# Optimization experiments

Measured on AMD Instinct MI355X. Metric: run time of the kernel, lower is better.

## Reference

```python
import jax, jax.numpy as jnp
import numpy as np

B, T, H, F = 32, 2048, 1024, 1024  # batch, kv_len, hidden_size, feature_size


def setup_inputs() -> dict:
    key = jax.random.key(0)
    ks = jax.random.split(key, 6)
    s = 0.02  # param init scale
    return {
        "query": jax.random.normal(ks[0], (B, 1, H), jnp.float32),
        "keys": jax.random.normal(ks[1], (B, T, F), jnp.float32),
        "Wa_w": jax.random.normal(ks[2], (H, H), jnp.float32) * s,
        "Wa_b": jnp.zeros((H,), jnp.float32),
        "Ua_w": jax.random.normal(ks[3], (H, F), jnp.float32) * s,
        "Ua_b": jnp.zeros((H,), jnp.float32),
        "Va_w": jax.random.normal(ks[4], (1, H), jnp.float32) * s,
        "Va_b": jnp.zeros((1,), jnp.float32),
    }


def reference(query, keys, Wa_w, Wa_b, Ua_w, Ua_b, Va_w, Va_b):
    # Wa(query): [B,1,H]; Ua(keys): [B,T,H]
    q = jnp.einsum('bqh,oh->bqo', query, Wa_w) + Wa_b
    k = jnp.einsum('btf,of->bto', keys, Ua_w) + Ua_b
    e = jnp.tanh(q + k)                                   # [B,T,H] (broadcast over q dim of size 1)
    scores = jnp.einsum('bth,h->bt', e, Va_w[0]) + Va_b[0]  # Va(...).squeeze(2) -> [B,T]
    scores = scores[:, None, :]                           # unsqueeze(1) -> [B,1,T]
    weights = jax.nn.softmax(scores, axis=-1)             # [B,1,T]
    context = jnp.einsum('bqt,btf->bqf', weights, keys)   # bmm -> [B,1,F]
    return context, weights
```

## Files before the change

kernel.cpp:

```cpp
#include <hip/hip_runtime.h>
#include <hip/hip_bf16.h>

typedef float  f32x4 __attribute__((ext_vector_type(4)));
typedef short  s16x8 __attribute__((ext_vector_type(8)));
typedef __hip_bfloat16 bf16;

#define BDIM 32
#define TDIM 2048
#define HDIM 1024
#define FDIM 1024
#define MTOT (BDIM*TDIM)

#define GLOAD16(gp, lp) __builtin_amdgcn_global_load_lds(                     \
    (const __attribute__((address_space(1))) void*)(gp),                      \
    (__attribute__((address_space(3))) void*)(lp), 16, 0, 0)

#define MFMA_BF16 __builtin_amdgcn_mfma_f32_16x16x32_bf16

__global__ __launch_bounds__(256) void cvt_bf16_kernel(
    const float* __restrict__ src, bf16* __restrict__ dst, int n8)
{
    int i = blockIdx.x * 256 + threadIdx.x;
    const int stride = gridDim.x * 256;
    for (; i < n8; i += stride) {
        const f32x4 a = ((const f32x4*)src)[2 * i];
        const f32x4 b = ((const f32x4*)src)[2 * i + 1];
        union { bf16 h[8]; s16x8 v; } u;
        #pragma unroll
        for (int j = 0; j < 4; ++j) {
            u.h[j]     = __float2bfloat16(a[j]);
            u.h[4 + j] = __float2bfloat16(b[j]);
        }
        ((s16x8*)dst)[i] = u.v;
    }
}

__global__ __launch_bounds__(256) void qeff_kernel(
    const float* __restrict__ query, const float* __restrict__ Wa_w,
    const float* __restrict__ Wa_b,  const float* __restrict__ Ua_b,
    float* __restrict__ qe)
{
    const int lane = threadIdx.x & 63;
    const int gw   = blockIdx.x * 4 + (threadIdx.x >> 6);
    const int b    = gw >> 10;
    const int o    = gw & 1023;
    const float* qp = query + (size_t)b * HDIM;
    const float* wp = Wa_w  + (size_t)o * HDIM;
    float s = 0.f;
    #pragma unroll
    for (int i = 0; i < 16; ++i) {
        const int h = i * 64 + lane;
        s += qp[h] * wp[h];
    }
    #pragma unroll
    for (int off = 32; off > 0; off >>= 1) s += __shfl_down(s, off);
    if (lane == 0) qe[gw] = s + Wa_b[o] + Ua_b[o];
}

#define STAGE_A(buf_, kb_, h_, s_) GLOAD16(                                    \
    Ab + (size_t)(M0 + (h_)*128 + (((s_)>>1)<<4) + srow) * FDIM               \
       + (kb_) + (((s_)&1)<<5) + scg*8,                                        \
    &As[buf_][((((h_)*8 + ((s_)>>1)) * 2 + ((s_)&1)) << 9)])
#define STAGE_B(buf_, kb_, h_, s_) GLOAD16(                                    \
    Bb + (size_t)(N0 + (h_)*128 + (((s_)>>1)<<4) + srow) * FDIM               \
       + (kb_) + (((s_)&1)<<5) + scg*8,                                        \
    &Bs[buf_][((((h_)*8 + ((s_)>>1)) * 2 + ((s_)&1)) << 9)])

__global__ __launch_bounds__(512) void score_gemm_256_kernel(
    const bf16* __restrict__ Ab, const bf16* __restrict__ Bb,
    const float* __restrict__ qe, const float* __restrict__ Va,
    float* __restrict__ scores)
{
    __shared__ bf16 As[2][16384];
    __shared__ bf16 Bs[2][16384];

    const int tid  = threadIdx.x;
    const int lane = tid & 63;
    const int w    = tid >> 6;
    const int wr   = w >> 2;
    const int wc   = w & 3;

    const int bid   = blockIdx.x;
    const int local = bid >> 3;
    const int mt    = (bid & 7) * 32 + (local >> 2);
    const int nt    = local & 3;
    const int M0 = mt * 256, N0 = nt * 256;

    const int srow = lane >> 2;
    const int scg  = (lane & 3) ^ (((lane >> 5) & 1) << 1);
    const int r    = lane & 15;
    const int q4   = lane >> 4;
    const int roff = r * 32 + ((q4 ^ (((r >> 3) & 1) << 1)) & 3) * 8;

    f32x4 acc[8][4];
    #pragma unroll
    for (int m = 0; m < 8; ++m)
        #pragma unroll
        for (int n = 0; n < 4; ++n) acc[m][n] = (f32x4){0.f, 0.f, 0.f, 0.f};

    STAGE_B(0, 0, 0, w); STAGE_B(0, 0, 0, w + 8);
    STAGE_B(0, 0, 1, w); STAGE_B(0, 0, 1, w + 8);
    STAGE_A(0, 0, 0, w); STAGE_A(0, 0, 0, w + 8);
    STAGE_A(0, 0, 1, w); STAGE_A(0, 0, 1, w + 8);
    STAGE_B(1, 64, 0, w); STAGE_B(1, 64, 0, w + 8);
    STAGE_B(1, 64, 1, w); STAGE_B(1, 64, 1, w + 8);
    asm volatile("s_waitcnt vmcnt(4)" ::: "memory");
    __builtin_amdgcn_s_barrier();

    for (int i = 0; i < 8; ++i) {
        const bool pf   = (i < 7);
        const int kbO1 = (2 * i + 1) << 6;
        const int kbE2 = (2 * i + 2) << 6;
        const int kbO2 = (2 * i + 3) << 6;

        s16x8 a0[4][2], a1[4][2], b0[2][2], b1[2][2];

        #pragma unroll
        for (int mf = 0; mf < 4; ++mf)
            #pragma unroll
            for (int ks = 0; ks < 2; ++ks)
                a0[mf][ks] = *(const s16x8*)
                    &As[0][(((wr * 8 + mf) * 2 + ks) << 9) + roff];
        #pragma unroll
        for (int nf = 0; nf < 2; ++nf)
            #pragma unroll
            for (int ks = 0; ks < 2; ++ks)
                b0[nf][ks] = *(const s16x8*)
                    &Bs[0][(((wc * 4 + nf) * 2 + ks) << 9) + roff];
        STAGE_A(1, kbO1, 0, w); STAGE_A(1, kbO1, 0, w + 8);
        __builtin_amdgcn_s_barrier();
        __builtin_amdgcn_s_setprio(1);
        #pragma unroll
        for (int mf = 0; mf < 4; ++mf)
            #pragma unroll
            for (int nf = 0; nf < 2; ++nf)
                #pragma unroll
                for (int ks = 0; ks < 2; ++ks)
                    acc[mf][nf] = MFMA_BF16(a0[mf][ks], b0[nf][ks],
                                            acc[mf][nf], 0, 0, 0);
        __builtin_amdgcn_s_setprio(0);
        __builtin_amdgcn_s_barrier();

        #pragma unroll
        for (int nf = 0; nf < 2; ++nf)
            #pragma unroll
            for (int ks = 0; ks < 2; ++ks)
                b1[nf][ks] = *(const s16x8*)
                    &Bs[0][(((wc * 4 + 2 + nf) * 2 + ks) << 9) + roff];
        STAGE_A(1, kbO1, 1, w); STAGE_A(1, kbO1, 1, w + 8);
        __builtin_amdgcn_s_barrier();
        __builtin_amdgcn_s_setprio(1);
        #pragma unroll
        for (int mf = 0; mf < 4; ++mf)
            #pragma unroll
            for (int nf = 0; nf < 2; ++nf)
                #pragma unroll
                for (int ks = 0; ks < 2; ++ks)
                    acc[mf][2 + nf] = MFMA_BF16(a0[mf][ks], b1[nf][ks],
                                                acc[mf][2 + nf], 0, 0, 0);
        __builtin_amdgcn_s_setprio(0);
        __builtin_amdgcn_s_barrier();

        #pragma unroll
        for (int mf = 0; mf < 4; ++mf)
            #pragma unroll
            for (int ks = 0; ks < 2; ++ks)
                a1[mf][ks] = *(const s16x8*)
                    &As[0][(((wr * 8 + 4 + mf) * 2 + ks) << 9) + roff];
        if (pf) { STAGE_B(0, kbE2, 0, w); STAGE_B(0, kbE2, 0, w + 8); }
        __builtin_amdgcn_s_barrier();
        __builtin_amdgcn_s_setprio(1);
        #pragma unroll
        for (int mf = 0; mf < 4; ++mf)
            #pragma unroll
            for (int nf = 0; nf < 2; ++nf)
                #pragma unroll
                for (int ks = 0; ks < 2; ++ks)
                    acc[4 + mf][nf] = MFMA_BF16(a1[mf][ks], b0[nf][ks],
                                                acc[4 + mf][nf], 0, 0, 0);
        __builtin_amdgcn_s_setprio(0);
        __builtin_amdgcn_s_barrier();

        if (pf) { STAGE_B(0, kbE2, 1, w); STAGE_B(0, kbE2, 1, w + 8); }
        __builtin_amdgcn_s_barrier();
        __builtin_amdgcn_s_setprio(1);
        #pragma unroll
        for (int mf = 0; mf < 4; ++mf)
            #pragma unroll
            for (int nf = 0; nf < 2; ++nf)
                #pragma unroll
                for (int ks = 0; ks < 2; ++ks)
                    acc[4 + mf][2 + nf] = MFMA_BF16(a1[mf][ks], b1[nf][ks],
                                                    acc[4 + mf][2 + nf], 0, 0, 0);
        __builtin_amdgcn_s_setprio(0);
        if (pf) asm volatile("s_waitcnt vmcnt(4)" ::: "memory");
        else    asm volatile("s_waitcnt vmcnt(0)" ::: "memory");
        __builtin_amdgcn_s_barrier();
        __builtin_amdgcn_sched_barrier(0);

        #pragma unroll
        for (int mf = 0; mf < 4; ++mf)
            #pragma unroll
            for (int ks = 0; ks < 2; ++ks)
                a0[mf][ks] = *(const s16x8*)
                    &As[1][(((wr * 8 + mf) * 2 + ks) << 9) + roff];
        #pragma unroll
        for (int nf = 0; nf < 2; ++nf)
            #pragma unroll
            for (int ks = 0; ks < 2; ++ks)
                b0[nf][ks] = *(const s16x8*)
                    &Bs[1][(((wc * 4 + nf) * 2 + ks) << 9) + roff];
        if (pf) { STAGE_A(0, kbE2, 0, w); STAGE_A(0, kbE2, 0, w + 8); }
        __builtin_amdgcn_s_barrier();
        __builtin_amdgcn_s_setprio(1);
        #pragma unroll
        for (int mf = 0; mf < 4; ++mf)
            #pragma unroll
            for (int nf = 0; nf < 2; ++nf)
                #pragma unroll
                for (int ks = 0; ks < 2; ++ks)
                    acc[mf][nf] = MFMA_BF16(a0[mf][ks], b0[nf][ks],
                                            acc[mf][nf], 0, 0, 0);
        __builtin_amdgcn_s_setprio(0);
        __builtin_amdgcn_s_barrier();

        #pragma unroll
        for (int nf = 0; nf < 2; ++nf)
            #pragma unroll
            for (int ks = 0; ks < 2; ++ks)
                b1[nf][ks] = *(const s16x8*)
                    &Bs[1][(((wc * 4 + 2 + nf) * 2 + ks) << 9) + roff];
        if (pf) { STAGE_A(0, kbE2, 1, w); STAGE_A(0, kbE2, 1, w + 8); }
        __builtin_amdgcn_s_barrier();
        __builtin_amdgcn_s_setprio(1);
        #pragma unroll
        for (int mf = 0; mf < 4; ++mf)
            #pragma unroll
            for (int nf = 0; nf < 2; ++nf)
                #pragma unroll
                for (int ks = 0; ks < 2; ++ks)
                    acc[mf][2 + nf] = MFMA_BF16(a0[mf][ks], b1[nf][ks],
                                                acc[mf][2 + nf], 0, 0, 0);
        __builtin_amdgcn_s_setprio(0);
        __builtin_amdgcn_s_barrier();

        #pragma unroll
        for (int mf = 0; mf < 4; ++mf)
            #pragma unroll
            for (int ks = 0; ks < 2; ++ks)
                a1[mf][ks] = *(const s16x8*)
                    &As[1][(((wr * 8 + 4 + mf) * 2 + ks) << 9) + roff];
        if (pf) { STAGE_B(1, kbO2, 0, w); STAGE_B(1, kbO2, 0, w + 8); }
        __builtin_amdgcn_s_barrier();
        __builtin_amdgcn_s_setprio(1);
        #pragma unroll
        for (int mf = 0; mf < 4; ++mf)
            #pragma unroll
            for (int nf = 0; nf < 2; ++nf)
                #pragma unroll
                for (int ks = 0; ks < 2; ++ks)
                    acc[4 + mf][nf] = MFMA_BF16(a1[mf][ks], b0[nf][ks],
                                                acc[4 + mf][nf], 0, 0, 0);
        __builtin_amdgcn_s_setprio(0);
        __builtin_amdgcn_s_barrier();

        if (pf) { STAGE_B(1, kbO2, 1, w); STAGE_B(1, kbO2, 1, w + 8); }
        __builtin_amdgcn_s_barrier();
        __builtin_amdgcn_s_setprio(1);
        #pragma unroll
        for (int mf = 0; mf < 4; ++mf)
            #pragma unroll
            for (int nf = 0; nf < 2; ++nf)
                #pragma unroll
                for (int ks = 0; ks < 2; ++ks)
                    acc[4 + mf][2 + nf] = MFMA_BF16(a1[mf][ks], b1[nf][ks],
                                                    acc[4 + mf][2 + nf], 0, 0, 0);
        __builtin_amdgcn_s_setprio(0);
        if (pf) {
            asm volatile("s_waitcnt vmcnt(4)" ::: "memory");
            __builtin_amdgcn_s_barrier();
            __builtin_amdgcn_sched_barrier(0);
        }
    }

    const int b = M0 >> 11;
    const float* qrow = qe + (size_t)b * HDIM;
    #pragma unroll
    for (int mf = 0; mf < 8; ++mf) {
        float part[4] = {0.f, 0.f, 0.f, 0.f};
        #pragma unroll
        for (int nf = 0; nf < 4; ++nf) {
            const int c    = N0 + wc * 64 + nf * 16 + (lane & 15);
            const float va = Va[c];
            const float qv = qrow[c];
            #pragma unroll
            for (int j = 0; j < 4; ++j) {
                const float x = qv + acc[mf][nf][j];
                const float e = __expf(2.0f * x);
                part[j] += va * (1.0f - 2.0f / (e + 1.0f));
            }
        }
        #pragma unroll
        for (int j = 0; j < 4; ++j)
            #pragma unroll
            for (int off = 1; off < 16; off <<= 1)
                part[j] += __shfl_xor(part[j], off);
        if ((lane & 15) == 0) {
            const int rr = M0 + wr * 128 + mf * 16 + (lane >> 4) * 4;
            #pragma unroll
            for (int j = 0; j < 4; ++j) atomicAdd(&scores[rr + j], part[j]);
        }
    }
}

__global__ __launch_bounds__(256) void score_gemm_f32_kernel(
    const float* __restrict__ keys, const float* __restrict__ Ua,
    const float* __restrict__ qe,   const float* __restrict__ Va,
    float* __restrict__ scores)
{
    __shared__ bf16 Asf[128][40];
    __shared__ bf16 Bsf[128][40];

    const int tid  = threadIdx.x;
    const int lane = tid & 63;
    const int wid  = tid >> 6;
    const int wr   = wid >> 1, wc = wid & 1;
    const int n0   = blockIdx.x * 128;
    const int m0   = blockIdx.y * 128;

    const int srow  = tid >> 1;
    const int shalf = tid & 1;
    const float* gA = keys + (size_t)(m0 + srow) * FDIM + shalf * 16;
    const float* gB = Ua   + (size_t)(n0 + srow) * FDIM + shalf * 16;

    f32x4 acc[4][4];
    #pragma unroll
    for (int m = 0; m < 4; ++m)
        #pragma unroll
        for (int n = 0; n < 4; ++n) acc[m][n] = (f32x4){0.f, 0.f, 0.f, 0.f};

    float4 ra[4], rbv[4];
    #pragma unroll
    for (int i = 0; i < 4; ++i) {
        ra[i]  = ((const float4*)gA)[i];
        rbv[i] = ((const float4*)gB)[i];
    }

    for (int kt = 0; kt < 32; ++kt) {
        __syncthreads();
        {
            union { bf16 h[16]; s16x8 v[2]; } ua, ub;
            #pragma unroll
            for (int i = 0; i < 4; ++i) {
                const float* fa = (const float*)&ra[i];
                const float* fb = (const float*)&rbv[i];
                #pragma unroll
                for (int j = 0; j < 4; ++j) {
                    ua.h[i*4+j] = __float2bfloat16(fa[j]);
                    ub.h[i*4+j] = __float2bfloat16(fb[j]);
                }
            }
            *(s16x8*)&Asf[srow][shalf*16]     = ua.v[0];
            *(s16x8*)&Asf[srow][shalf*16 + 8] = ua.v[1];
            *(s16x8*)&Bsf[srow][shalf*16]     = ub.v[0];
            *(s16x8*)&Bsf[srow][shalf*16 + 8] = ub.v[1];
        }
        __syncthreads();

        if (kt + 1 < 32) {
            const float* pa = gA + (kt + 1) * 32;
            const float* pb = gB + (kt + 1) * 32;
            #pragma unroll
            for (int i = 0; i < 4; ++i) {
                ra[i]  = ((const float4*)pa)[i];
                rbv[i] = ((const float4*)pb)[i];
            }
        }

        s16x8 af[4], bfr[4];
        #pragma unroll
        for (int m = 0; m < 4; ++m)
            af[m] = *(const s16x8*)&Asf[wr*64 + m*16 + (lane & 15)][(lane >> 4) * 8];
        #pragma unroll
        for (int n = 0; n < 4; ++n)
            bfr[n] = *(const s16x8*)&Bsf[wc*64 + n*16 + (lane & 15)][(lane >> 4) * 8];
        #pragma unroll
        for (int m = 0; m < 4; ++m)
            #pragma unroll
            for (int n = 0; n < 4; ++n)
                acc[m][n] = MFMA_BF16(af[m], bfr[n], acc[m][n], 0, 0, 0);
    }

    const int b = m0 >> 11;
    const float* qrow = qe + (size_t)b * HDIM;
    #pragma unroll
    for (int m = 0; m < 4; ++m) {
        float part[4] = {0.f, 0.f, 0.f, 0.f};
        #pragma unroll
        for (int n = 0; n < 4; ++n) {
            const int c    = n0 + wc*64 + n*16 + (lane & 15);
            const float va = Va[c];
            const float qv = qrow[c];
            #pragma unroll
            for (int j = 0; j < 4; ++j) {
                const float x = qv + acc[m][n][j];
                const float e = __expf(2.0f * x);
                part[j] += va * (1.0f - 2.0f / (e + 1.0f));
            }
        }
        #pragma unroll
        for (int j = 0; j < 4; ++j)
            #pragma unroll
            for (int off = 1; off < 16; off <<= 1)
                part[j] += __shfl_xor(part[j], off);
        if ((lane & 15) == 0) {
            const int rr = m0 + wr*64 + m*16 + (lane >> 4) * 4;
            #pragma unroll
            for (int j = 0; j < 4; ++j) atomicAdd(&scores[rr + j], part[j]);
        }
    }
}

__global__ __launch_bounds__(256) void softmax_kernel(float* __restrict__ sw)
{
    const int b    = blockIdx.x;
    const int tid  = threadIdx.x;
    const int lane = tid & 63, wid = tid >> 6;
    __shared__ float red[8];

    float v[8];
    float m = -3.4e38f;
    #pragma unroll
    for (int i = 0; i < 8; ++i) {
        v[i] = sw[b * TDIM + i * 256 + tid];
        m = fmaxf(m, v[i]);
    }
    #pragma unroll
    for (int off = 32; off > 0; off >>= 1) m = fmaxf(m, __shfl_xor(m, off));
    if (lane == 0) red[wid] = m;
    __syncthreads();
    m = fmaxf(fmaxf(red[0], red[1]), fmaxf(red[2], red[3]));

    float s = 0.f;
    #pragma unroll
    for (int i = 0; i < 8; ++i) { v[i] = __expf(v[i] - m); s += v[i]; }
    #pragma unroll
    for (int off = 32; off > 0; off >>= 1) s += __shfl_xor(s, off);
    if (lane == 0) red[4 + wid] = s;
    __syncthreads();
    s = (red[4] + red[5]) + (red[6] + red[7]);

    const float inv = 1.0f / s;
    #pragma unroll
    for (int i = 0; i < 8; ++i) sw[b * TDIM + i * 256 + tid] = v[i] * inv;
}

__global__ __launch_bounds__(256) void context_bf16_kernel(
    const bf16* __restrict__ keys, const float* __restrict__ w,
    float* __restrict__ ctx)
{
    const int tc  = blockIdx.x;
    const int b   = blockIdx.y;
    const int tid = threadIdx.x;
    __shared__ float ws_[128];
    if (tid < 128) ws_[tid] = w[b * TDIM + tc * 128 + tid];
    __syncthreads();

    const bf16* kp = keys + ((size_t)b * TDIM + (size_t)tc * 128) * FDIM + tid * 4;
    float4 acc = {0.f, 0.f, 0.f, 0.f};
    #pragma unroll 8
    for (int t = 0; t < 128; ++t) {
        const short4 kv = *(const short4*)(kp + (size_t)t * FDIM);
        const float wt = ws_[t];
        acc.x += wt * __uint_as_float(((unsigned)(unsigned short)kv.x) << 16);
        acc.y += wt * __uint_as_float(((unsigned)(unsigned short)kv.y) << 16);
        acc.z += wt * __uint_as_float(((unsigned)(unsigned short)kv.z) << 16);
        acc.w += wt * __uint_as_float(((unsigned)(unsigned short)kv.w) << 16);
    }
    float* cp = ctx + (size_t)b * FDIM + tid * 4;
    atomicAdd(cp + 0, acc.x); atomicAdd(cp + 1, acc.y);
    atomicAdd(cp + 2, acc.z); atomicAdd(cp + 3, acc.w);
}

__global__ __launch_bounds__(256) void context_f32_kernel(
    const float* __restrict__ keys, const float* __restrict__ w,
    float* __restrict__ ctx)
{
    const int tc  = blockIdx.x;
    const int b   = blockIdx.y;
    const int tid = threadIdx.x;
    __shared__ float ws_[128];
    if (tid < 128) ws_[tid] = w[b * TDIM + tc * 128 + tid];
    __syncthreads();

    const float* kp = keys + ((size_t)b * TDIM + (size_t)tc * 128) * FDIM + tid * 4;
    float4 acc = {0.f, 0.f, 0.f, 0.f};
    #pragma unroll 8
    for (int t = 0; t < 128; ++t) {
        const float4 kv = *(const float4*)(kp + (size_t)t * FDIM);
        const float wt = ws_[t];
        acc.x += wt * kv.x; acc.y += wt * kv.y;
        acc.z += wt * kv.z; acc.w += wt * kv.w;
    }
    float* cp = ctx + (size_t)b * FDIM + tid * 4;
    atomicAdd(cp + 0, acc.x); atomicAdd(cp + 1, acc.y);
    atomicAdd(cp + 2, acc.z); atomicAdd(cp + 3, acc.w);
}

extern "C" void kernel_launch(void* const* d_in, const int* in_sizes, int n_in,
                              void* d_out, int out_size, void* d_ws, size_t ws_size,
                              hipStream_t stream)
{
    const float* query = (const float*)d_in[0];
    const float* keys  = (const float*)d_in[1];
    const float* Wa_w  = (const float*)d_in[2];
    const float* Wa_b  = (const float*)d_in[3];
    const float* Ua_w  = (const float*)d_in[4];
    const float* Ua_b  = (const float*)d_in[5];
    const float* Va_w  = (const float*)d_in[6];

    float* out = (float*)d_out;
    float* ctx = out;
    float* sw  = out + BDIM * HDIM;

    const size_t needA = (size_t)MTOT * FDIM * sizeof(bf16);
    const size_t needB = (size_t)HDIM * FDIM * sizeof(bf16);
    const bool fast = ws_size >= needA + needB;

    hipMemsetAsync(sw, 0, (size_t)BDIM * TDIM * sizeof(float), stream);
    qeff_kernel<<<dim3(BDIM * HDIM / 4), 256, 0, stream>>>(query, Wa_w, Wa_b, Ua_b, ctx);

    if (fast) {
        bf16* Ab = (bf16*)d_ws;
        bf16* Bb = Ab + (size_t)MTOT * FDIM;
        cvt_bf16_kernel<<<dim3(2048), 256, 0, stream>>>(keys, Ab, MTOT * FDIM / 8);
        cvt_bf16_kernel<<<dim3(512),  256, 0, stream>>>(Ua_w, Bb, HDIM * FDIM / 8);
        score_gemm_256_kernel<<<dim3(1024), 512, 0, stream>>>(Ab, Bb, ctx, Va_w, sw);
        softmax_kernel<<<dim3(BDIM), 256, 0, stream>>>(sw);
        hipMemsetAsync(ctx, 0, (size_t)BDIM * HDIM * sizeof(float), stream);
        context_bf16_kernel<<<dim3(16, BDIM), 256, 0, stream>>>(Ab, sw, ctx);
    } else {
        score_gemm_f32_kernel<<<dim3(HDIM / 128, MTOT / 128), 256, 0, stream>>>(
            keys, Ua_w, ctx, Va_w, sw);
        softmax_kernel<<<dim3(BDIM), 256, 0, stream>>>(sw);
        hipMemsetAsync(ctx, 0, (size_t)BDIM * HDIM * sizeof(float), stream);
        context_f32_kernel<<<dim3(16, BDIM), 256, 0, stream>>>(keys, sw, ctx);
    }
}
```

Baseline: 271.5 us.

## Loop each GEMM block over all N tiles and replace atomics with partial buffers

The score GEMM now launches 256 blocks, each owning one 256-row M tile and looping over all four 256-column N tiles. The next tile's initial loads are prefetched during the tanh/Va epilogue. Per-tile row partial scores are reduced across waves in shared memory and written to a 4-slice partial buffer, which removes the global atomics and the scores memset. A new softmax kernel sums the four partials. The cost is that only 256 blocks run, roughly one per CU, so occupancy and latency hiding drop, and the workspace needs room for the partial buffer.

New measurement: 271.9 us. Within noise of the previous version (+0.1%).

```diff
diff --git a/kernel.cpp b/kernel.cpp
--- a/kernel.cpp
+++ b/kernel.cpp
@@ -61,18 +61,19 @@
     Ab + (size_t)(M0 + (h_)*128 + (((s_)>>1)<<4) + srow) * FDIM               \
        + (kb_) + (((s_)&1)<<5) + scg*8,                                        \
     &As[buf_][((((h_)*8 + ((s_)>>1)) * 2 + ((s_)&1)) << 9)])
-#define STAGE_B(buf_, kb_, h_, s_) GLOAD16(                                    \
-    Bb + (size_t)(N0 + (h_)*128 + (((s_)>>1)<<4) + srow) * FDIM               \
+#define STAGE_B(buf_, n0_, kb_, h_, s_) GLOAD16(                               \
+    Bb + (size_t)((n0_) + (h_)*128 + (((s_)>>1)<<4) + srow) * FDIM            \
        + (kb_) + (((s_)&1)<<5) + scg*8,                                        \
     &Bs[buf_][((((h_)*8 + ((s_)>>1)) * 2 + ((s_)&1)) << 9)])
 
 __global__ __launch_bounds__(512) void score_gemm_256_kernel(
     const bf16* __restrict__ Ab, const bf16* __restrict__ Bb,
     const float* __restrict__ qe, const float* __restrict__ Va,
-    float* __restrict__ scores)
+    float* __restrict__ part_out)
 {
     __shared__ bf16 As[2][16384];
     __shared__ bf16 Bs[2][16384];
+    __shared__ float red[4][256];
 
     const int tid  = threadIdx.x;
     const int lane = tid & 63;
@@ -80,11 +81,9 @@
     const int wr   = w >> 2;
     const int wc   = w & 3;
 
-    const int bid   = blockIdx.x;
-    const int local = bid >> 3;
-    const int mt    = (bid & 7) * 32 + (local >> 2);
-    const int nt    = local & 3;
-    const int M0 = mt * 256, N0 = nt * 256;
+    const int bid = blockIdx.x;
+    const int mt  = (bid & 7) * 32 + (bid >> 3);
+    const int M0  = mt * 256;
 
     const int srow = lane >> 2;
     const int scg  = (lane & 3) ^ (((lane >> 5) & 1) << 1);
@@ -92,223 +91,250 @@
     const int q4   = lane >> 4;
     const int roff = r * 32 + ((q4 ^ (((r >> 3) & 1) << 1)) & 3) * 8;
 
-    f32x4 acc[8][4];
-    #pragma unroll
-    for (int m = 0; m < 8; ++m)
-        #pragma unroll
-        for (int n = 0; n < 4; ++n) acc[m][n] = (f32x4){0.f, 0.f, 0.f, 0.f};
-
-    STAGE_B(0, 0, 0, w); STAGE_B(0, 0, 0, w + 8);
-    STAGE_B(0, 0, 1, w); STAGE_B(0, 0, 1, w + 8);
+    const int bb = M0 >> 11;
+    const float* qrow = qe + (size_t)bb * HDIM;
+
+    STAGE_B(0, 0, 0, 0, w); STAGE_B(0, 0, 0, 0, w + 8);
+    STAGE_B(0, 0, 0, 1, w); STAGE_B(0, 0, 0, 1, w + 8);
     STAGE_A(0, 0, 0, w); STAGE_A(0, 0, 0, w + 8);
     STAGE_A(0, 0, 1, w); STAGE_A(0, 0, 1, w + 8);
-    STAGE_B(1, 64, 0, w); STAGE_B(1, 64, 0, w + 8);
-    STAGE_B(1, 64, 1, w); STAGE_B(1, 64, 1, w + 8);
-    asm volatile("s_waitcnt vmcnt(4)" ::: "memory");
-    __builtin_amdgcn_s_barrier();
-
-    for (int i = 0; i < 8; ++i) {
-        const bool pf   = (i < 7);
-        const int kbO1 = (2 * i + 1) << 6;
-        const int kbE2 = (2 * i + 2) << 6;
-        const int kbO2 = (2 * i + 3) << 6;
-
-        s16x8 a0[4][2], a1[4][2], b0[2][2], b1[2][2];
-
-        #pragma unroll
-        for (int mf = 0; mf < 4; ++mf)
-            #pragma unroll
-            for (int ks = 0; ks < 2; ++ks)
-                a0[mf][ks] = *(const s16x8*)
-                    &As[0][(((wr * 8 + mf) * 2 + ks) << 9) + roff];
-        #pragma unroll
-        for (int nf = 0; nf < 2; ++nf)
-            #pragma unroll
-            for (int ks = 0; ks < 2; ++ks)
-                b0[nf][ks] = *(const s16x8*)
-                    &Bs[0][(((wc * 4 + nf) * 2 + ks) << 9) + roff];
-        STAGE_A(1, kbO1, 0, w); STAGE_A(1, kbO1, 0, w + 8);
-        __builtin_amdgcn_s_barrier();
-        __builtin_amdgcn_s_setprio(1);
-        #pragma unroll
-        for (int mf = 0; mf < 4; ++mf)
-            #pragma unroll
-            for (int nf = 0; nf < 2; ++nf)
-                #pragma unroll
-                for (int ks = 0; ks < 2; ++ks)
-                    acc[mf][nf] = MFMA_BF16(a0[mf][ks], b0[nf][ks],
-                                            acc[mf][nf], 0, 0, 0);
-        __builtin_amdgcn_s_setprio(0);
-        __builtin_amdgcn_s_barrier();
-
-        #pragma unroll
-        for (int nf = 0; nf < 2; ++nf)
-            #pragma unroll
-            for (int ks = 0; ks < 2; ++ks)
-                b1[nf][ks] = *(const s16x8*)
-                    &Bs[0][(((wc * 4 + 2 + nf) * 2 + ks) << 9) + roff];
-        STAGE_A(1, kbO1, 1, w); STAGE_A(1, kbO1, 1, w + 8);
-        __builtin_amdgcn_s_barrier();
-        __builtin_amdgcn_s_setprio(1);
-        #pragma unroll
-        for (int mf = 0; mf < 4; ++mf)
-            #pragma unroll
-            for (int nf = 0; nf < 2; ++nf)
-                #pragma unroll
-                for (int ks = 0; ks < 2; ++ks)
-                    acc[mf][2 + nf] = MFMA_BF16(a0[mf][ks], b1[nf][ks],
-                                                acc[mf][2 + nf], 0, 0, 0);
-        __builtin_amdgcn_s_setprio(0);
-        __builtin_amdgcn_s_barrier();
-
-        #pragma unroll
-        for (int mf = 0; mf < 4; ++mf)
-            #pragma unroll
-            for (int ks = 0; ks < 2; ++ks)
-                a1[mf][ks] = *(const s16x8*)
-                    &As[0][(((wr * 8 + 4 + mf) * 2 + ks) << 9) + roff];
-        if (pf) { STAGE_B(0, kbE2, 0, w); STAGE_B(0, kbE2, 0, w + 8); }
-        __builtin_amdgcn_s_barrier();
-        __builtin_amdgcn_s_setprio(1);
-        #pragma unroll
-        for (int mf = 0; mf < 4; ++mf)
-            #pragma unroll
-            for (int nf = 0; nf < 2; ++nf)
-                #pragma unroll
-                for (int ks = 0; ks < 2; ++ks)
-                    acc[4 + mf][nf] = MFMA_BF16(a1[mf][ks], b0[nf][ks],
-                                                acc[4 + mf][nf], 0, 0, 0);
-        __builtin_amdgcn_s_setprio(0);
-        __builtin_amdgcn_s_barrier();
-
-        if (pf) { STAGE_B(0, kbE2, 1, w); STAGE_B(0, kbE2, 1, w + 8); }
-        __builtin_amdgcn_s_barrier();
-        __builtin_amdgcn_s_setprio(1);
-        #pragma unroll
-        for (int mf = 0; mf < 4; ++mf)
-            #pragma unroll
-            for (int nf = 0; nf < 2; ++nf)
-                #pragma unroll
-                for (int ks = 0; ks < 2; ++ks)
-                    acc[4 + mf][2 + nf] = MFMA_BF16(a1[mf][ks], b1[nf][ks],
-                                                    acc[4 + mf][2 + nf], 0, 0, 0);
-        __builtin_amdgcn_s_setprio(0);
-        if (pf) asm volatile("s_waitcnt vmcnt(4)" ::: "memory");
-        else    asm volatile("s_waitcnt vmcnt(0)" ::: "memory");
+    STAGE_B(1, 0, 64, 0, w); STAGE_B(1, 0, 64, 0, w + 8);
+    STAGE_B(1, 0, 64, 1, w); STAGE_B(1, 0, 64, 1, w + 8);
+
+    for (int g = 0; g < 4; ++g) {
+        const int N0 = g << 8;
+
+        asm volatile("s_waitcnt vmcnt(4)" ::: "memory");
         __builtin_amdgcn_s_barrier();
         __builtin_amdgcn_sched_barrier(0);
 
-        #pragma unroll
-        for (int mf = 0; mf < 4; ++mf)
-            #pragma unroll
-            for (int ks = 0; ks < 2; ++ks)
-                a0[mf][ks] = *(const s16x8*)
-                    &As[1][(((wr * 8 + mf) * 2 + ks) << 9) + roff];
-        #pragma unroll
-        for (int nf = 0; nf < 2; ++nf)
-            #pragma unroll
-            for (int ks = 0; ks < 2; ++ks)
-                b0[nf][ks] = *(const s16x8*)
-                    &Bs[1][(((wc * 4 + nf) * 2 + ks) << 9) + roff];
-        if (pf) { STAGE_A(0, kbE2, 0, w); STAGE_A(0, kbE2, 0, w + 8); }
+        f32x4 acc[8][4];
+        #pragma unroll
+        for (int m = 0; m < 8; ++m)
+            #pragma unroll
+            for (int n = 0; n < 4; ++n) acc[m][n] = (f32x4){0.f, 0.f, 0.f, 0.f};
+
+        for (int i = 0; i < 8; ++i) {
+            const bool pf  = (i < 7);
+            const int kbO1 = (2 * i + 1) << 6;
+            const int kbE2 = (2 * i + 2) << 6;
+            const int kbO2 = (2 * i + 3) << 6;
+
+            s16x8 a0[4][2], a1[4][2], b0[2][2], b1[2][2];
+
+            #pragma unroll
+            for (int mf = 0; mf < 4; ++mf)
+                #pragma unroll
+                for (int ks = 0; ks < 2; ++ks)
+                    a0[mf][ks] = *(const s16x8*)
+                        &As[0][(((wr * 8 + mf) * 2 + ks) << 9) + roff];
+            #pragma unroll
+            for (int nf = 0; nf < 2; ++nf)
+                #pragma unroll
+                for (int ks = 0; ks < 2; ++ks)
+                    b0[nf][ks] = *(const s16x8*)
+                        &Bs[0][(((wc * 4 + nf) * 2 + ks) << 9) + roff];
+            STAGE_A(1, kbO1, 0, w); STAGE_A(1, kbO1, 0, w + 8);
+            __builtin_amdgcn_s_barrier();
+            __builtin_amdgcn_s_setprio(1);
+            #pragma unroll
+            for (int mf = 0; mf < 4; ++mf)
+                #pragma unroll
+                for (int nf = 0; nf < 2; ++nf)
+                    #pragma unroll
+                    for (int ks = 0; ks < 2; ++ks)
+                        acc[mf][nf] = MFMA_BF16(a0[mf][ks], b0[nf][ks],
+                                                acc[mf][nf], 0, 0, 0);
+            __builtin_amdgcn_s_setprio(0);
+            __builtin_amdgcn_s_barrier();
+
+            #pragma unroll
+            for (int nf = 0; nf < 2; ++nf)
+                #pragma unroll
+                for (int ks = 0; ks < 2; ++ks)
+                    b1[nf][ks] = *(const s16x8*)
+                        &Bs[0][(((wc * 4 + 2 + nf) * 2 + ks) << 9) + roff];
+            STAGE_A(1, kbO1, 1, w); STAGE_A(1, kbO1, 1, w + 8);
+            __builtin_amdgcn_s_barrier();
+            __builtin_amdgcn_s_setprio(1);
+            #pragma unroll
+            for (int mf = 0; mf < 4; ++mf)
+                #pragma unroll
+                for (int nf = 0; nf < 2; ++nf)
+                    #pragma unroll
+                    for (int ks = 0; ks < 2; ++ks)
+                        acc[mf][2 + nf] = MFMA_BF16(a0[mf][ks], b1[nf][ks],
+                                                    acc[mf][2 + nf], 0, 0, 0);
+            __builtin_amdgcn_s_setprio(0);
+            __builtin_amdgcn_s_barrier();
+
+            #pragma unroll
+            for (int mf = 0; mf < 4; ++mf)
+                #pragma unroll
+                for (int ks = 0; ks < 2; ++ks)
+                    a1[mf][ks] = *(const s16x8*)
+                        &As[0][(((wr * 8 + 4 + mf) * 2 + ks) << 9) + roff];
+            if (pf) { STAGE_B(0, N0, kbE2, 0, w); STAGE_B(0, N0, kbE2, 0, w + 8); }
+            __builtin_amdgcn_s_barrier();
+            __builtin_amdgcn_s_setprio(1);
+            #pragma unroll
+            for (int mf = 0; mf < 4; ++mf)
+                #pragma unroll
+                for (int nf = 0; nf < 2; ++nf)
+                    #pragma unroll
+                    for (int ks = 0; ks < 2; ++ks)
+                        acc[4 + mf][nf] = MFMA_BF16(a1[mf][ks], b0[nf][ks],
+                                                    acc[4 + mf][nf], 0, 0, 0);
+            __builtin_amdgcn_s_setprio(0);
+            __builtin_amdgcn_s_barrier();
+
+            if (pf) { STAGE_B(0, N0, kbE2, 1, w); STAGE_B(0, N0, kbE2, 1, w + 8); }
+            __builtin_amdgcn_s_barrier();
+            __builtin_amdgcn_s_setprio(1);
+            #pragma unroll
+            for (int mf = 0; mf < 4; ++mf)
+                #pragma unroll
+                for (int nf = 0; nf < 2; ++nf)
+                    #pragma unroll
+                    for (int ks = 0; ks < 2; ++ks)
+                        acc[4 + mf][2 + nf] = MFMA_BF16(a1[mf][ks], b1[nf][ks],
+                                                        acc[4 + mf][2 + nf], 0, 0, 0);
+            __builtin_amdgcn_s_setprio(0);
+            if (pf) asm volatile("s_waitcnt vmcnt(4)" ::: "memory");
+            else    asm volatile("s_waitcnt vmcnt(0)" ::: "memory");
+            __builtin_amdgcn_s_barrier();
+            __builtin_amdgcn_sched_barrier(0);
+
+            #pragma unroll
+            for (int mf = 0; mf < 4; ++mf)
+                #pragma unroll
+                for (int ks = 0; ks < 2; ++ks)
+                    a0[mf][ks] = *(const s16x8*)
+                        &As[1][(((wr * 8 + mf) * 2 + ks) << 9) + roff];
+            #pragma unroll
+            for (int nf = 0; nf < 2; ++nf)
+                #pragma unroll
+                for (int ks = 0; ks < 2; ++ks)
+                    b0[nf][ks] = *(const s16x8*)
+                        &Bs[1][(((wc * 4 + nf) * 2 + ks) << 9) + roff];
+            if (pf) { STAGE_A(0, kbE2, 0, w); STAGE_A(0, kbE2, 0, w + 8); }
+            __builtin_amdgcn_s_barrier();
+            __builtin_amdgcn_s_setprio(1);
+            #pragma unroll
+            for (int mf = 0; mf < 4; ++mf)
+                #pragma unroll
+                for (int nf = 0; nf < 2; ++nf)
+                    #pragma unroll
+                    for (int ks = 0; ks < 2; ++ks)
+                        acc[mf][nf] = MFMA_BF16(a0[mf][ks], b0[nf][ks],
+                                                acc[mf][nf], 0, 0, 0);
+            __builtin_amdgcn_s_setprio(0);
+            __builtin_amdgcn_s_barrier();
+
+            #pragma unroll
+            for (int nf = 0; nf < 2; ++nf)
+                #pragma unroll
+                for (int ks = 0; ks < 2; ++ks)
+                    b1[nf][ks] = *(const s16x8*)
+                        &Bs[1][(((wc * 4 + 2 + nf) * 2 + ks) << 9) + roff];
+            if (pf) { STAGE_A(0, kbE2, 1, w); STAGE_A(0, kbE2, 1, w + 8); }
+            __builtin_amdgcn_s_barrier();
+            __builtin_amdgcn_s_setprio(1);
+            #pragma unroll
+            for (int mf = 0; mf < 4; ++mf)
+                #pragma unroll
+                for (int nf = 0; nf < 2; ++nf)
+                    #pragma unroll
+                    for (int ks = 0; ks < 2; ++ks)
+                        acc[mf][2 + nf] = MFMA_BF16(a0[mf][ks], b1[nf][ks],
+                                                    acc[mf][2 + nf], 0, 0, 0);
+            __builtin_amdgcn_s_setprio(0);
+            __builtin_amdgcn_s_barrier();
+
+            #pragma unroll
+            for (int mf = 0; mf < 4; ++mf)
+                #pragma unroll
+                for (int ks = 0; ks < 2; ++ks)
+                    a1[mf][ks] = *(const s16x8*)
+                        &As[1][(((wr * 8 + 4 + mf) * 2 + ks) << 9) + roff];
+            if (pf) { STAGE_B(1, N0, kbO2, 0, w); STAGE_B(1, N0, kbO2, 0, w + 8); }
+            __builtin_amdgcn_s_barrier();
+            __builtin_amdgcn_s_setprio(1);
+            #pragma unroll
+            for (int mf = 0; mf < 4; ++mf)
+                #pragma unroll
+                for (int nf = 0; nf < 2; ++nf)
+                    #pragma unroll
+                    for (int ks = 0; ks < 2; ++ks)
+                        acc[4 + mf][nf] = MFMA_BF16(a1[mf][ks], b0[nf][ks],
+                                                    acc[4 + mf][nf], 0, 0, 0);
+            __builtin_amdgcn_s_setprio(0);
+            __builtin_amdgcn_s_barrier();
+
+            if (pf) { STAGE_B(1, N0, kbO2, 1, w); STAGE_B(1, N0, kbO2, 1, w + 8); }
+            __builtin_amdgcn_s_barrier();
+            __builtin_amdgcn_s_setprio(1);
+            #pragma unroll
+            for (int mf = 0; mf < 4; ++mf)
+                #pragma unroll
+                for (int nf = 0; nf < 2; ++nf)
+                    #pragma unroll
+                    for (int ks = 0; ks < 2; ++ks)
+                        acc[4 + mf][2 + nf] = MFMA_BF16(a1[mf][ks], b1[nf][ks],
+                                                        acc[4 + mf][2 + nf], 0, 0, 0);
+            __builtin_amdgcn_s_setprio(0);
+            if (pf) {
+                asm volatile("s_waitcnt vmcnt(4)" ::: "memory");
+                __builtin_amdgcn_s_barrier();
+                __builtin_amdgcn_sched_barrier(0);
+            }
+        }
+
         __builtin_amdgcn_s_barrier();
-        __builtin_amdgcn_s_setprio(1);
-        #pragma unroll
-        for (int mf = 0; mf < 4; ++mf)
-            #pragma unroll
-            for (int nf = 0; nf < 2; ++nf)
-                #pragma unroll
-                for (int ks = 0; ks < 2; ++ks)
-                    acc[mf][nf] = MFMA_BF16(a0[mf][ks], b0[nf][ks],
-                                            acc[mf][nf], 0, 0, 0);
-        __builtin_amdgcn_s_setprio(0);
+
+        if (g < 3) {
+            const int n0n = (g + 1) << 8;
+            STAGE_B(0, n0n, 0, 0, w); STAGE_B(0, n0n, 0, 0, w + 8);
+            STAGE_B(0, n0n, 0, 1, w); STAGE_B(0, n0n, 0, 1, w + 8);
+            STAGE_A(0, 0, 0, w); STAGE_A(0, 0, 0, w + 8);
+            STAGE_A(0, 0, 1, w); STAGE_A(0, 0, 1, w + 8);
+            STAGE_B(1, n0n, 64, 0, w); STAGE_B(1, n0n, 64, 0, w + 8);
+            STAGE_B(1, n0n, 64, 1, w); STAGE_B(1, n0n, 64, 1, w + 8);
+        }
+
+        #pragma unroll
+        for (int mf = 0; mf < 8; ++mf) {
+            float part[4] = {0.f, 0.f, 0.f, 0.f};
+            #pragma unroll
+            for (int nf = 0; nf < 4; ++nf) {
+                const int c    = N0 + wc * 64 + nf * 16 + (lane & 15);
+                const float va = Va[c];
+                const float qv = qrow[c];
+                #pragma unroll
+                for (int j = 0; j < 4; ++j) {
+                    const float x = qv + acc[mf][nf][j];
+                    const float e = __expf(2.0f * x);
+                    part[j] += va * (1.0f - 2.0f / (e + 1.0f));
+                }
+            }
+            #pragma unroll
+            for (int j = 0; j < 4; ++j)
+                #pragma unroll
+                for (int off = 1; off < 16; off <<= 1)
+                    part[j] += __shfl_xor(part[j], off);
+            if ((lane & 15) == 0) {
+                const int row = wr * 128 + mf * 16 + q4 * 4;
+                float4 pv = {part[0], part[1], part[2], part[3]};
+                *(float4*)&red[wc][row] = pv;
+            }
+        }
+        asm volatile("s_waitcnt lgkmcnt(0)" ::: "memory");
         __builtin_amdgcn_s_barrier();
 
-        #pragma unroll
-        for (int nf = 0; nf < 2; ++nf)
-            #pragma unroll
-            for (int ks = 0; ks < 2; ++ks)
-                b1[nf][ks] = *(const s16x8*)
-                    &Bs[1][(((wc * 4 + 2 + nf) * 2 + ks) << 9) + roff];
-        if (pf) { STAGE_A(0, kbE2, 1, w); STAGE_A(0, kbE2, 1, w + 8); }
-        __builtin_amdgcn_s_barrier();
-        __builtin_amdgcn_s_setprio(1);
-        #pragma unroll
-        for (int mf = 0; mf < 4; ++mf)
-            #pragma unroll
-            for (int nf = 0; nf < 2; ++nf)
-                #pragma unroll
-                for (int ks = 0; ks < 2; ++ks)
-                    acc[mf][2 + nf] = MFMA_BF16(a0[mf][ks], b1[nf][ks],
-                                                acc[mf][2 + nf], 0, 0, 0);
-        __builtin_amdgcn_s_setprio(0);
-        __builtin_amdgcn_s_barrier();
-
-        #pragma unroll
-        for (int mf = 0; mf < 4; ++mf)
-            #pragma unroll
-            for (int ks = 0; ks < 2; ++ks)
-                a1[mf][ks] = *(const s16x8*)
-                    &As[1][(((wr * 8 + 4 + mf) * 2 + ks) << 9) + roff];
-        if (pf) { STAGE_B(1, kbO2, 0, w); STAGE_B(1, kbO2, 0, w + 8); }
-        __builtin_amdgcn_s_barrier();
-        __builtin_amdgcn_s_setprio(1);
-        #pragma unroll
-        for (int mf = 0; mf < 4; ++mf)
-            #pragma unroll
-            for (int nf = 0; nf < 2; ++nf)
-                #pragma unroll
-                for (int ks = 0; ks < 2; ++ks)
-                    acc[4 + mf][nf] = MFMA_BF16(a1[mf][ks], b0[nf][ks],
-                                                acc[4 + mf][nf], 0, 0, 0);
-        __builtin_amdgcn_s_setprio(0);
-        __builtin_amdgcn_s_barrier();
-
-        if (pf) { STAGE_B(1, kbO2, 1, w); STAGE_B(1, kbO2, 1, w + 8); }
-        __builtin_amdgcn_s_barrier();
-        __builtin_amdgcn_s_setprio(1);
-        #pragma unroll
-        for (int mf = 0; mf < 4; ++mf)
-            #pragma unroll
-            for (int nf = 0; nf < 2; ++nf)
-                #pragma unroll
-                for (int ks = 0; ks < 2; ++ks)
-                    acc[4 + mf][2 + nf] = MFMA_BF16(a1[mf][ks], b1[nf][ks],
-                                                    acc[4 + mf][2 + nf], 0, 0, 0);
-        __builtin_amdgcn_s_setprio(0);
-        if (pf) {
-            asm volatile("s_waitcnt vmcnt(4)" ::: "memory");
-            __builtin_amdgcn_s_barrier();
-            __builtin_amdgcn_sched_barrier(0);
-        }
-    }
-
-    const int b = M0 >> 11;
-    const float* qrow = qe + (size_t)b * HDIM;
-    #pragma unroll
-    for (int mf = 0; mf < 8; ++mf) {
-        float part[4] = {0.f, 0.f, 0.f, 0.f};
-        #pragma unroll
-        for (int nf = 0; nf < 4; ++nf) {
-            const int c    = N0 + wc * 64 + nf * 16 + (lane & 15);
-            const float va = Va[c];
-            const float qv = qrow[c];
-            #pragma unroll
-            for (int j = 0; j < 4; ++j) {
-                const float x = qv + acc[mf][nf][j];
-                const float e = __expf(2.0f * x);
-                part[j] += va * (1.0f - 2.0f / (e + 1.0f));
-            }
-        }
-        #pragma unroll
-        for (int j = 0; j < 4; ++j)
-            #pragma unroll
-            for (int off = 1; off < 16; off <<= 1)
-                part[j] += __shfl_xor(part[j], off);
-        if ((lane & 15) == 0) {
-            const int rr = M0 + wr * 128 + mf * 16 + (lane >> 4) * 4;
-            #pragma unroll
-            for (int j = 0; j < 4; ++j) atomicAdd(&scores[rr + j], part[j]);
+        if (tid < 256) {
+            const float s4 = (red[0][tid] + red[1][tid])
+                           + (red[2][tid] + red[3][tid]);
+            part_out[(size_t)g * MTOT + M0 + tid] = s4;
         }
     }
 }
@@ -419,6 +445,43 @@
             for (int j = 0; j < 4; ++j) atomicAdd(&scores[rr + j], part[j]);
         }
     }
+}
+
+__global__ __launch_bounds__(256) void softmax_partial_kernel(
+    const float* __restrict__ part, float* __restrict__ sw)
+{
+    const int b    = blockIdx.x;
+    const int tid  = threadIdx.x;
+    const int lane = tid & 63, wid = tid >> 6;
+    __shared__ float red[8];
+
+    float v[8];
+    float m = -3.4e38f;
+    #pragma unroll
+    for (int i = 0; i < 8; ++i) {
+        const size_t idx = (size_t)b * TDIM + i * 256 + tid;
+        v[i] = (part[idx] + part[idx + MTOT])
+             + (part[idx + 2 * (size_t)MTOT] + part[idx + 3 * (size_t)MTOT]);
+        m = fmaxf(m, v[i]);
+    }
+    #pragma unroll
+    for (int off = 32; off > 0; off >>= 1) m = fmaxf(m, __shfl_xor(m, off));
+    if (lane == 0) red[wid] = m;
+    __syncthreads();
+    m = fmaxf(fmaxf(red[0], red[1]), fmaxf(red[2], red[3]));
+
+    float s = 0.f;
+    #pragma unroll
+    for (int i = 0; i < 8; ++i) { v[i] = __expf(v[i] - m); s += v[i]; }
+    #pragma unroll
+    for (int off = 32; off > 0; off >>= 1) s += __shfl_xor(s, off);
+    if (lane == 0) red[4 + wid] = s;
+    __syncthreads();
+    s = (red[4] + red[5]) + (red[6] + red[7]);
+
+    const float inv = 1.0f / s;
+    #pragma unroll
+    for (int i = 0; i < 8; ++i) sw[b * TDIM + i * 256 + tid] = v[i] * inv;
 }
 
 __global__ __launch_bounds__(256) void softmax_kernel(float* __restrict__ sw)
@@ -525,21 +588,23 @@
 
     const size_t needA = (size_t)MTOT * FDIM * sizeof(bf16);
     const size_t needB = (size_t)HDIM * FDIM * sizeof(bf16);
-    const bool fast = ws_size >= needA + needB;
-
-    hipMemsetAsync(sw, 0, (size_t)BDIM * TDIM * sizeof(float), stream);
+    const size_t needP = (size_t)4 * MTOT * sizeof(float);
+    const bool fast = ws_size >= needA + needB + needP;
+
     qeff_kernel<<<dim3(BDIM * HDIM / 4), 256, 0, stream>>>(query, Wa_w, Wa_b, Ua_b, ctx);
 
     if (fast) {
-        bf16* Ab = (bf16*)d_ws;
-        bf16* Bb = Ab + (size_t)MTOT * FDIM;
+        bf16*  Ab      = (bf16*)d_ws;
+        bf16*  Bb      = Ab + (size_t)MTOT * FDIM;
+        float* partial = (float*)(Bb + (size_t)HDIM * FDIM);
         cvt_bf16_kernel<<<dim3(2048), 256, 0, stream>>>(keys, Ab, MTOT * FDIM / 8);
         cvt_bf16_kernel<<<dim3(512),  256, 0, stream>>>(Ua_w, Bb, HDIM * FDIM / 8);
-        score_gemm_256_kernel<<<dim3(1024), 512, 0, stream>>>(Ab, Bb, ctx, Va_w, sw);
-        softmax_kernel<<<dim3(BDIM), 256, 0, stream>>>(sw);
+        score_gemm_256_kernel<<<dim3(256), 512, 0, stream>>>(Ab, Bb, ctx, Va_w, partial);
+        softmax_partial_kernel<<<dim3(BDIM), 256, 0, stream>>>(partial, sw);
         hipMemsetAsync(ctx, 0, (size_t)BDIM * HDIM * sizeof(float), stream);
         context_bf16_kernel<<<dim3(16, BDIM), 256, 0, stream>>>(Ab, sw, ctx);
     } else {
+        hipMemsetAsync(sw, 0, (size_t)BDIM * TDIM * sizeof(float), stream);
         score_gemm_f32_kernel<<<dim3(HDIM / 128, MTOT / 128), 256, 0, stream>>>(
             keys, Ua_w, ctx, Va_w, sw);
         softmax_kernel<<<dim3(BDIM), 256, 0, stream>>>(sw);
```
